# Performance work log

Hardware: AMD Instinct MI355X
Metric: run time of the kernel (lower is better)

Reference implementation:

```python
import jax, jax.numpy as jnp
import numpy as np

N_NODES = 50000
N_EDGES = 800000
IN_CH = 128
HEADS = 4
OUT_CH = 32
NEG_SLOPE = 0.2


def setup_inputs() -> dict:
    key = jax.random.key(0)
    ks = jax.random.split(key, 8)
    x = jax.random.normal(ks[0], (N_NODES, IN_CH), dtype=jnp.float32)
    # edges guaranteed to have no self-loops (module removes then re-adds them)
    tgt = jax.random.randint(ks[1], (N_EDGES,), 0, N_NODES)
    off = jax.random.randint(ks[2], (N_EDGES,), 1, N_NODES)
    src = (tgt + off) % N_NODES
    edge_index = jnp.stack([src, tgt]).astype(jnp.int64)
    glorot = lambda k, shp: jax.random.uniform(
        k, shp, jnp.float32, -1.0, 1.0) * np.sqrt(6.0 / (shp[-1] + shp[-2]))
    Wl = glorot(ks[3], (HEADS * OUT_CH, IN_CH))  # torch Linear weight [out,in]
    Wr = glorot(ks[4], (HEADS * OUT_CH, IN_CH))
    att = glorot(ks[5], (1, HEADS, OUT_CH))
    bl = jnp.zeros((HEADS * OUT_CH,), jnp.float32)
    br = jnp.zeros((HEADS * OUT_CH,), jnp.float32)
    bias = jnp.zeros((HEADS * OUT_CH,), jnp.float32)
    return {"x": x, "edge_index": edge_index, "Wl": Wl, "bl": bl,
            "Wr": Wr, "br": br, "att": att, "bias": bias}


def _forward(x, edge_index, Wl, bl, Wr, br, att, bias):
    H, C = HEADS, OUT_CH
    n = x.shape[0]
    x_l = (x @ Wl.T + bl).reshape(n, H, C)  # target projection
    x_r = (x @ Wr.T + br).reshape(n, H, C)  # source projection
    # add self-loops (inputs contain none by construction)
    loops = jnp.arange(n, dtype=edge_index.dtype)
    src = jnp.concatenate([edge_index[0], loops])
    tgt = jnp.concatenate([edge_index[1], loops])
    x_i = x_l[tgt]                     # [E', H, C]
    x_j = x_r[src]                     # [E', H, C]
    a_in = jax.nn.leaky_relu(x_i + x_j, NEG_SLOPE)
    alpha = jnp.einsum('ehc,ohc->eh', a_in, att)  # [E', H]
    # segment softmax over target nodes
    m = jax.ops.segment_max(alpha, tgt, num_segments=n)
    alpha = jnp.exp(alpha - jax.lax.stop_gradient(m)[tgt])
    denom = jax.ops.segment_sum(alpha, tgt, num_segments=n)
    alpha = alpha / denom[tgt]
    msgs = x_j * alpha[:, :, None]     # [E', H, C]
    out = jax.ops.segment_sum(msgs, tgt, num_segments=n)  # [N, H, C]
    out = out.reshape(n, H * C) + bias  # concat=True
    return out


def reference(x, edge_index, Wl, bl, Wr, br, att, bias):
    return _forward(x, edge_index, Wl, bl, Wr, br, att, bias)
```

## Files before the change

### kernel.cpp

```cpp
#include <hip/hip_runtime.h>
#include <hip/hip_bf16.h>
#include <stdint.h>

#define N_NODES 50000
#define N_EDGES 800000
#define IN_CH   128
#define NEG_SLOPE 0.2f

#define E_PER 8
#define FILL_BLOCKS 391

typedef short short8 __attribute__((ext_vector_type(8)));
typedef float f32x4  __attribute__((ext_vector_type(4)));
typedef float f32x2  __attribute__((ext_vector_type(2)));

static __device__ __forceinline__ float bf_lo(uint32_t p) { return __uint_as_float(p << 16); }
static __device__ __forceinline__ float bf_hi(uint32_t p) { return __uint_as_float(p & 0xffff0000u); }
static __device__ __forceinline__ uint16_t f_to_bf(float f) {
    uint32_t u = __float_as_uint(f);
    u += 0x7fffu + ((u >> 16) & 1u);
    return (uint16_t)(u >> 16);
}

static __device__ __forceinline__ f32x2 lrelu2(f32x2 x) {
    f32x2 s = x * NEG_SLOPE;
    f32x2 r;
    r[0] = fmaxf(x[0], s[0]);
    r[1] = fmaxf(x[1], s[1]);
    return r;
}

static __device__ __forceinline__ float sum16(float x) {
    x += __uint_as_float(__builtin_amdgcn_update_dpp(0, __float_as_uint(x), 0xB1,  0xf, 0xf, true));
    x += __uint_as_float(__builtin_amdgcn_update_dpp(0, __float_as_uint(x), 0x4E,  0xf, 0xf, true));
    x += __uint_as_float(__builtin_amdgcn_update_dpp(0, __float_as_uint(x), 0x141, 0xf, 0xf, true));
    x += __uint_as_float(__builtin_amdgcn_update_dpp(0, __float_as_uint(x), 0x140, 0xf, 0xf, true));
    return x;
}

static __device__ __forceinline__ void sum16x2(float& a, float& b) {
    asm("s_nop 0\n\t"
        "v_add_f32 %0, %0, %0 quad_perm:[1,0,3,2] row_mask:0xf bank_mask:0xf bound_ctrl:0\n\t"
        "v_add_f32 %1, %1, %1 quad_perm:[1,0,3,2] row_mask:0xf bank_mask:0xf bound_ctrl:0\n\t"
        "v_add_f32 %0, %0, %0 quad_perm:[2,3,0,1] row_mask:0xf bank_mask:0xf bound_ctrl:0\n\t"
        "v_add_f32 %1, %1, %1 quad_perm:[2,3,0,1] row_mask:0xf bank_mask:0xf bound_ctrl:0\n\t"
        "v_add_f32 %0, %0, %0 row_half_mirror row_mask:0xf bank_mask:0xf bound_ctrl:0\n\t"
        "v_add_f32 %1, %1, %1 row_half_mirror row_mask:0xf bank_mask:0xf bound_ctrl:0\n\t"
        "v_add_f32 %0, %0, %0 row_mirror row_mask:0xf bank_mask:0xf bound_ctrl:0\n\t"
        "v_add_f32 %1, %1, %1 row_mirror row_mask:0xf bank_mask:0xf bound_ctrl:0"
        : "+v"(a), "+v"(b));
}

__global__ __launch_bounds__(256) void prep_kernel(
    const float* __restrict__ Wl, const float* __restrict__ Wr,
    __hip_bfloat16* __restrict__ wswz, int* __restrict__ cnt)
{
    int t = blockIdx.x * 256 + threadIdx.x;
    if (t < 4096) {
        int ct = t >> 8, rem = t & 255;
        int ch = rem >> 6, lane = rem & 63;
        int m = lane & 15, quad = lane >> 4;
        const float* W = (ct < 8) ? Wl : Wr;
        int o = ((ct & 7) << 4) + m;
        const float* src = W + (size_t)o * IN_CH + ch * 32 + quad * 8;
        short8 f;
#pragma unroll
        for (int j = 0; j < 8; ++j) f[j] = (short)f_to_bf(src[j]);
        *(short8*)((short*)wswz + (size_t)t * 8) = f;
    }
    for (int i = t; i < N_NODES; i += 64 * 256) cnt[i] = 0;
}

__global__ __launch_bounds__(256) void fill_kernel(
    const int* __restrict__ ei, int cap,
    int* __restrict__ cnt, uint16_t* __restrict__ csr)
{
    const uint32_t* eiw = (const uint32_t*)ei;
    bool z = (eiw[2 * (threadIdx.x & 63) + 1] == 0u);
    bool is64 = __popcll(__ballot(z)) >= 32;

    int tid = blockIdx.x * 256 + threadIdx.x;
    int e0 = tid * E_PER;
    if (e0 >= N_EDGES) return;

    int src[E_PER], tgt[E_PER];
    if (is64) {
        const int4* ps = (const int4*)(eiw + 2 * (size_t)e0);
        const int4* pt = (const int4*)(eiw + 2 * ((size_t)N_EDGES + e0));
#pragma unroll
        for (int k = 0; k < 4; ++k) {
            int4 s = ps[k], t = pt[k];
            src[2 * k] = s.x; src[2 * k + 1] = s.z;
            tgt[2 * k] = t.x; tgt[2 * k + 1] = t.z;
        }
    } else {
        const int4* ps = (const int4*)(ei + e0);
        const int4* pt = (const int4*)(ei + N_EDGES + e0);
#pragma unroll
        for (int k = 0; k < 2; ++k) {
            int4 s = ps[k], t = pt[k];
            src[4 * k] = s.x; src[4 * k + 1] = s.y; src[4 * k + 2] = s.z; src[4 * k + 3] = s.w;
            tgt[4 * k] = t.x; tgt[4 * k + 1] = t.y; tgt[4 * k + 2] = t.z; tgt[4 * k + 3] = t.w;
        }
    }

    int pos[E_PER];
#pragma unroll
    for (int k = 0; k < E_PER; ++k) {
        bool ok = (unsigned)src[k] < N_NODES && (unsigned)tgt[k] < N_NODES;
        pos[k] = ok ? atomicAdd(&cnt[tgt[k]], 1) : cap;
    }
#pragma unroll
    for (int k = 0; k < E_PER; ++k)
        if (pos[k] < cap) csr[(size_t)tgt[k] * cap + pos[k]] = (uint16_t)src[k];
}

__global__ __launch_bounds__(256) void proj_kernel(
    const float* __restrict__ x, const __hip_bfloat16* __restrict__ wswz,
    const float* __restrict__ bl, const float* __restrict__ br,
    float* __restrict__ xl, __hip_bfloat16* __restrict__ xr)
{
    int rowbase = blockIdx.x * 16;
    int lane = threadIdx.x & 63;
    int widx = threadIdx.x >> 6;
    int m = lane & 15;
    int quad = lane >> 4;

    short8 afrag[4];
    const float* xrow = x + (size_t)(rowbase + m) * IN_CH;
#pragma unroll
    for (int ch = 0; ch < 4; ++ch) {
        f32x4 p0 = *(const f32x4*)(xrow + ch * 32 + quad * 8);
        f32x4 p1 = *(const f32x4*)(xrow + ch * 32 + quad * 8 + 4);
        short8 f;
#pragma unroll
        for (int j = 0; j < 4; ++j) { f[j] = (short)f_to_bf(p0[j]); f[j + 4] = (short)f_to_bf(p1[j]); }
        afrag[ch] = f;
    }

    const short* wz = (const short*)wswz;
    const float* bv = (widx < 2) ? bl : br;
#pragma unroll
    for (int cc = 0; cc < 4; ++cc) {
        int ct = widx * 4 + cc;
        int o = ((ct & 7) << 4) + m;
        f32x4 acc = {0.f, 0.f, 0.f, 0.f};
#pragma unroll
        for (int ch = 0; ch < 4; ++ch) {
            short8 bfrag = *(const short8*)(wz + ((size_t)(ct * 4 + ch) * 64 + lane) * 8);
            acc = __builtin_amdgcn_mfma_f32_16x16x32_bf16(afrag[ch], bfrag, acc, 0, 0, 0);
        }
        float bias_v = bv[o];
        if (widx < 2) {
#pragma unroll
            for (int r = 0; r < 4; ++r)
                xl[(size_t)(rowbase + quad * 4 + r) * IN_CH + o] = acc[r] + bias_v;
        } else {
#pragma unroll
            for (int r = 0; r < 4; ++r)
                xr[(size_t)(rowbase + quad * 4 + r) * IN_CH + o] = __float2bfloat16(acc[r] + bias_v);
        }
    }
}

__global__ __launch_bounds__(256) void agg_kernel(
    const __hip_bfloat16* __restrict__ xr,
    const int* __restrict__ cnt, const uint16_t* __restrict__ csr, int cap,
    const float* __restrict__ att, const float* __restrict__ bias,
    float* out )
{
    int n = blockIdx.x * 4 + (threadIdx.x >> 6);
    if (n >= N_NODES) return;
    int lane = threadIdx.x & 63;

    const uint32_t* xrw = (const uint32_t*)xr;

    f32x2 qv = *(const f32x2*)(out + (size_t)n * IN_CH + 2 * lane);
    f32x2 av = *(const f32x2*)(att + 2 * lane);
    f32x2 bv = *(const f32x2*)(bias + 2 * lane);

    int deg = min(cnt[n], cap);
    const uint16_t* lst = csr + (size_t)n * cap;
    int idxreg = (int)lst[min(lane, cap - 1)];

    uint32_t u = xrw[(size_t)n * 64 + lane];
    f32x2 a0v; a0v[0] = bf_lo(u); a0v[1] = bf_hi(u);
    f32x2 p0 = lrelu2(qv + a0v) * av;
    float t = sum16(p0[0] + p0[1]);
    float w = __expf(t);
    float lsum = w;
    f32x2 acc = w * a0v;

    if (deg > 0) {
        int dm1 = deg - 1;
        int s0a = __builtin_amdgcn_readlane(idxreg, 0);
        int s0b = __builtin_amdgcn_readlane(idxreg, min(1, dm1));
        int s1a = __builtin_amdgcn_readlane(idxreg, min(2, dm1));
        int s1b = __builtin_amdgcn_readlane(idxreg, min(3, dm1));
        uint32_t uA0 = xrw[(size_t)s0a * 64 + lane];
        uint32_t uB0 = xrw[(size_t)s0b * 64 + lane];
        uint32_t uA1 = xrw[(size_t)s1a * 64 + lane];
        uint32_t uB1 = xrw[(size_t)s1b * 64 + lane];
        int i = 0;
        while (i + 1 < deg) {
            int s2a = __builtin_amdgcn_readlane(idxreg, min(i + 4, dm1));
            int s2b = __builtin_amdgcn_readlane(idxreg, min(i + 5, dm1));
            uint32_t uA2 = xrw[(size_t)s2a * 64 + lane];
            uint32_t uB2 = xrw[(size_t)s2b * 64 + lane];

            f32x2 aA; aA[0] = bf_lo(uA0); aA[1] = bf_hi(uA0);
            f32x2 aB; aB[0] = bf_lo(uB0); aB[1] = bf_hi(uB0);
            f32x2 pA = lrelu2(qv + aA) * av;
            f32x2 pB = lrelu2(qv + aB) * av;
            float tA = pA[0] + pA[1];
            float tB = pB[0] + pB[1];
            sum16x2(tA, tB);
            float wA = __expf(tA), wB = __expf(tB);
            lsum += wA + wB;
            acc += wA * aA;
            acc += wB * aB;

            uA0 = uA1; uB0 = uB1;
            uA1 = uA2; uB1 = uB2;
            i += 2;
        }
        if (i < deg) {
            f32x2 aA; aA[0] = bf_lo(uA0); aA[1] = bf_hi(uA0);
            f32x2 pA = lrelu2(qv + aA) * av;
            float tA = sum16(pA[0] + pA[1]);
            float wA = __expf(tA);
            lsum += wA;
            acc += wA * aA;
        }
    }

    float inv = 1.f / lsum;
    f32x2 ov = acc * inv + bv;
    *(f32x2*)(out + (size_t)n * IN_CH + 2 * lane) = ov;
}

extern "C" void kernel_launch(void* const* d_in, const int* in_sizes, int n_in,
                              void* d_out, int out_size, void* d_ws, size_t ws_size,
                              hipStream_t stream) {
    const float* x    = (const float*)d_in[0];
    const int*   ei   = (const int*)d_in[1];
    const float* Wl   = (const float*)d_in[2];
    const float* bl   = (const float*)d_in[3];
    const float* Wr   = (const float*)d_in[4];
    const float* br   = (const float*)d_in[5];
    const float* att  = (const float*)d_in[6];
    const float* bias = (const float*)d_in[7];
    float* out = (float*)d_out;

    const size_t CSR_BASE = 13065536;
    char* ws = (char*)d_ws;
    __hip_bfloat16* xr   = (__hip_bfloat16*)(ws);
    __hip_bfloat16* wswz = (__hip_bfloat16*)(ws + 12800000);
    int*      cnt = (int*)(ws + 12865536);
    uint16_t* csr = (uint16_t*)(ws + CSR_BASE);

    long long avail = (ws_size > CSR_BASE) ? (long long)(ws_size - CSR_BASE) : 0;
    int cap = (int)(avail / ((long long)N_NODES * 2));
    if (cap > 64) cap = 64;
    if (cap < 1)  cap = 1;

    prep_kernel<<<64, 256, 0, stream>>>(Wl, Wr, wswz, cnt);
    fill_kernel<<<FILL_BLOCKS, 256, 0, stream>>>(ei, cap, cnt, csr);
    proj_kernel<<<N_NODES / 16, 256, 0, stream>>>(x, wswz, bl, br, out, xr);
    agg_kernel<<<N_NODES / 4, 256, 0, stream>>>(xr, cnt, csr, cap, att, bias, out);
}
```

Measured before the change: 190.9 us.

## Build CSR via bucketed two-pass sort fused with projection kernel

Replaces the global-atomic scatter CSR fill with a two-level bucket sort. Edges are histogrammed into 512-node buckets in shared memory and written to per-bucket regions, then a per-bucket kernel builds a compact CSR slab with packed 8-bit degrees in LDS. The fill blocks are fused into the projection kernel launch, so edge bucketing overlaps with the MFMA projection and one launch goes away. This aims to cut scattered global atomics and uncoalesced CSR writes. In exchange it needs extra workspace, caps per-bucket and per-node counts (BCAP, CAPR=48) that could drop edges on skewed graphs, and keeps the old path as a fallback.

```diff
diff --git a/kernel.cpp b/kernel.cpp
--- a/kernel.cpp
+++ b/kernel.cpp
@@ -6,6 +6,13 @@
 #define N_EDGES 800000
 #define IN_CH   128
 #define NEG_SLOPE 0.2f
+
+#define NBUCK   98
+#define E1      8000
+#define FILLB   100
+#define BCAP    12288
+#define BSTRIDE 49152
+#define CAPR    48
 
 #define E_PER 8
 #define FILL_BLOCKS 391
@@ -51,24 +58,176 @@
         : "+v"(a), "+v"(b));
 }
 
+static __device__ __forceinline__ void wswz_body(
+    int t, const float* __restrict__ Wl, const float* __restrict__ Wr,
+    __hip_bfloat16* __restrict__ wswz)
+{
+    int ct = t >> 8, rem = t & 255;
+    int ch = rem >> 6, lane = rem & 63;
+    int m = lane & 15, quad = lane >> 4;
+    const float* W = (ct < 8) ? Wl : Wr;
+    int o = ((ct & 7) << 4) + m;
+    const float* src = W + (size_t)o * IN_CH + ch * 32 + quad * 8;
+    short8 f;
+#pragma unroll
+    for (int j = 0; j < 8; ++j) f[j] = (short)f_to_bf(src[j]);
+    *(short8*)((short*)wswz + (size_t)t * 8) = f;
+}
+
+static __device__ __forceinline__ void proj_body(
+    int rowbase, int tid,
+    const float* __restrict__ x, const __hip_bfloat16* __restrict__ wswz,
+    const float* __restrict__ bl, const float* __restrict__ br,
+    float* __restrict__ xl, __hip_bfloat16* __restrict__ xr)
+{
+    int lane = tid & 63;
+    int widx = tid >> 6;
+    int m = lane & 15;
+    int quad = lane >> 4;
+
+    short8 afrag[4];
+    const float* xrow = x + (size_t)(rowbase + m) * IN_CH;
+#pragma unroll
+    for (int ch = 0; ch < 4; ++ch) {
+        f32x4 p0 = *(const f32x4*)(xrow + ch * 32 + quad * 8);
+        f32x4 p1 = *(const f32x4*)(xrow + ch * 32 + quad * 8 + 4);
+        short8 f;
+#pragma unroll
+        for (int j = 0; j < 4; ++j) { f[j] = (short)f_to_bf(p0[j]); f[j + 4] = (short)f_to_bf(p1[j]); }
+        afrag[ch] = f;
+    }
+
+    const short* wz = (const short*)wswz;
+    const float* bv = (widx < 2) ? bl : br;
+#pragma unroll
+    for (int cc = 0; cc < 4; ++cc) {
+        int ct = widx * 4 + cc;
+        int o = ((ct & 7) << 4) + m;
+        f32x4 acc = {0.f, 0.f, 0.f, 0.f};
+#pragma unroll
+        for (int ch = 0; ch < 4; ++ch) {
+            short8 bfrag = *(const short8*)(wz + ((size_t)(ct * 4 + ch) * 64 + lane) * 8);
+            acc = __builtin_amdgcn_mfma_f32_16x16x32_bf16(afrag[ch], bfrag, acc, 0, 0, 0);
+        }
+        float bias_v = bv[o];
+        if (widx < 2) {
+#pragma unroll
+            for (int r = 0; r < 4; ++r)
+                xl[(size_t)(rowbase + quad * 4 + r) * IN_CH + o] = acc[r] + bias_v;
+        } else {
+#pragma unroll
+            for (int r = 0; r < 4; ++r)
+                xr[(size_t)(rowbase + quad * 4 + r) * IN_CH + o] = __float2bfloat16(acc[r] + bias_v);
+        }
+    }
+}
+
 __global__ __launch_bounds__(256) void prep_kernel(
     const float* __restrict__ Wl, const float* __restrict__ Wr,
-    __hip_bfloat16* __restrict__ wswz, int* __restrict__ cnt)
+    __hip_bfloat16* __restrict__ wswz, int* __restrict__ z, int zn)
 {
     int t = blockIdx.x * 256 + threadIdx.x;
-    if (t < 4096) {
-        int ct = t >> 8, rem = t & 255;
-        int ch = rem >> 6, lane = rem & 63;
-        int m = lane & 15, quad = lane >> 4;
-        const float* W = (ct < 8) ? Wl : Wr;
-        int o = ((ct & 7) << 4) + m;
-        const float* src = W + (size_t)o * IN_CH + ch * 32 + quad * 8;
-        short8 f;
-#pragma unroll
-        for (int j = 0; j < 8; ++j) f[j] = (short)f_to_bf(src[j]);
-        *(short8*)((short*)wswz + (size_t)t * 8) = f;
-    }
-    for (int i = t; i < N_NODES; i += 64 * 256) cnt[i] = 0;
+    if (t < 4096) wswz_body(t, Wl, Wr, wswz);
+    for (int i = t; i < zn; i += 64 * 256) z[i] = 0;
+}
+
+__global__ __launch_bounds__(256) void proj_fill(
+    const float* __restrict__ x, const __hip_bfloat16* __restrict__ wswz,
+    const float* __restrict__ bl, const float* __restrict__ br,
+    float* __restrict__ xl, __hip_bfloat16* __restrict__ xr,
+    const int* __restrict__ ei, uint32_t* __restrict__ bcnt,
+    char* __restrict__ region)
+{
+    __shared__ uint32_t s_sorted[E1];
+    __shared__ uint32_t s_hist[NBUCK], s_lstart[NBUCK], s_loc[NBUCK], s_gbase[NBUCK];
+    __shared__ uint32_t s_T;
+
+    if (blockIdx.x >= FILLB) {
+        proj_body((blockIdx.x - FILLB) * 16, threadIdx.x, x, wswz, bl, br, xl, xr);
+        return;
+    }
+
+    int tid = threadIdx.x;
+    int fb = blockIdx.x;
+    for (int i = tid; i < NBUCK; i += 256) s_hist[i] = 0;
+    __syncthreads();
+
+    const uint32_t* eiw = (const uint32_t*)ei;
+    bool zlo = (eiw[2 * (tid & 63) + 1] == 0u);
+    bool is64 = __popcll(__ballot(zlo)) >= 32;
+    int e0 = fb * E1;
+
+    for (int k = tid; k < E1; k += 256) {
+        int e = e0 + k;
+        int s = is64 ? (int)eiw[2 * (size_t)e] : ei[e];
+        int t = is64 ? (int)eiw[2 * ((size_t)N_EDGES + e)] : ei[N_EDGES + e];
+        if ((unsigned)s < N_NODES && (unsigned)t < N_NODES)
+            atomicAdd(&s_hist[t >> 9], 1u);
+    }
+    __syncthreads();
+
+    if (tid < NBUCK) s_gbase[tid] = atomicAdd(&bcnt[tid], s_hist[tid]);
+    if (tid == 0) {
+        uint32_t acc = 0;
+        for (int i = 0; i < NBUCK; ++i) { s_lstart[i] = acc; acc += s_hist[i]; }
+        s_T = acc;
+    }
+    __syncthreads();
+    if (tid < NBUCK) s_loc[tid] = s_lstart[tid];
+    __syncthreads();
+
+    for (int k = tid; k < E1; k += 256) {
+        int e = e0 + k;
+        int s = is64 ? (int)eiw[2 * (size_t)e] : ei[e];
+        int t = is64 ? (int)eiw[2 * ((size_t)N_EDGES + e)] : ei[N_EDGES + e];
+        if ((unsigned)s < N_NODES && (unsigned)t < N_NODES) {
+            uint32_t r = atomicAdd(&s_loc[t >> 9], 1u);
+            s_sorted[r] = ((uint32_t)t << 16) | (uint32_t)s;
+        }
+    }
+    __syncthreads();
+
+    int T = (int)s_T;
+    for (int k = tid; k < T; k += 256) {
+        uint32_t v = s_sorted[k];
+        uint32_t key = v >> 25;
+        uint32_t g = s_gbase[key] + (uint32_t)k - s_lstart[key];
+        if (g < BCAP)
+            ((uint32_t*)(region + (size_t)key * BSTRIDE))[g] = v;
+    }
+}
+
+__global__ __launch_bounds__(256) void csr_build(
+    const uint32_t* __restrict__ bcnt, char* __restrict__ region,
+    uint32_t* __restrict__ degs32)
+{
+    __shared__ uint16_t slab[512 * CAPR];
+    __shared__ uint32_t lcnt[512];
+    int b = blockIdx.x, tid = threadIdx.x;
+    for (int i = tid; i < 512; i += 256) lcnt[i] = 0;
+    __syncthreads();
+
+    uint32_t* reg = (uint32_t*)(region + (size_t)b * BSTRIDE);
+    int M = min((int)bcnt[b], BCAP);
+    for (int k = tid; k < M; k += 256) {
+        uint32_t v = reg[k];
+        int node = (int)((v >> 16) & 511u);
+        uint32_t pos = atomicAdd(&lcnt[node], 1u);
+        if (pos < CAPR) slab[node * CAPR + pos] = (uint16_t)(v & 0xffffu);
+    }
+    __syncthreads();
+
+    const uint32_t* sw = (const uint32_t*)slab;
+    for (int j = tid; j < (512 * CAPR / 2); j += 256) reg[j] = sw[j];
+    if (tid < 128) {
+        uint32_t p = 0;
+#pragma unroll
+        for (int q = 0; q < 4; ++q) {
+            uint32_t d = min(lcnt[tid * 4 + q], (uint32_t)CAPR);
+            p |= d << (q * 8);
+        }
+        degs32[b * 128 + tid] = p;
+    }
 }
 
 __global__ __launch_bounds__(256) void fill_kernel(
@@ -120,52 +279,13 @@
     const float* __restrict__ bl, const float* __restrict__ br,
     float* __restrict__ xl, __hip_bfloat16* __restrict__ xr)
 {
-    int rowbase = blockIdx.x * 16;
-    int lane = threadIdx.x & 63;
-    int widx = threadIdx.x >> 6;
-    int m = lane & 15;
-    int quad = lane >> 4;
-
-    short8 afrag[4];
-    const float* xrow = x + (size_t)(rowbase + m) * IN_CH;
-#pragma unroll
-    for (int ch = 0; ch < 4; ++ch) {
-        f32x4 p0 = *(const f32x4*)(xrow + ch * 32 + quad * 8);
-        f32x4 p1 = *(const f32x4*)(xrow + ch * 32 + quad * 8 + 4);
-        short8 f;
-#pragma unroll
-        for (int j = 0; j < 4; ++j) { f[j] = (short)f_to_bf(p0[j]); f[j + 4] = (short)f_to_bf(p1[j]); }
-        afrag[ch] = f;
-    }
-
-    const short* wz = (const short*)wswz;
-    const float* bv = (widx < 2) ? bl : br;
-#pragma unroll
-    for (int cc = 0; cc < 4; ++cc) {
-        int ct = widx * 4 + cc;
-        int o = ((ct & 7) << 4) + m;
-        f32x4 acc = {0.f, 0.f, 0.f, 0.f};
-#pragma unroll
-        for (int ch = 0; ch < 4; ++ch) {
-            short8 bfrag = *(const short8*)(wz + ((size_t)(ct * 4 + ch) * 64 + lane) * 8);
-            acc = __builtin_amdgcn_mfma_f32_16x16x32_bf16(afrag[ch], bfrag, acc, 0, 0, 0);
-        }
-        float bias_v = bv[o];
-        if (widx < 2) {
-#pragma unroll
-            for (int r = 0; r < 4; ++r)
-                xl[(size_t)(rowbase + quad * 4 + r) * IN_CH + o] = acc[r] + bias_v;
-        } else {
-#pragma unroll
-            for (int r = 0; r < 4; ++r)
-                xr[(size_t)(rowbase + quad * 4 + r) * IN_CH + o] = __float2bfloat16(acc[r] + bias_v);
-        }
-    }
+    proj_body(blockIdx.x * 16, threadIdx.x, x, wswz, bl, br, xl, xr);
 }
 
 __global__ __launch_bounds__(256) void agg_kernel(
     const __hip_bfloat16* __restrict__ xr,
-    const int* __restrict__ cnt, const uint16_t* __restrict__ csr, int cap,
+    const char* __restrict__ degbase, int degpacked,
+    const uint16_t* __restrict__ csr, int ldcsr, int cap,
     const float* __restrict__ att, const float* __restrict__ bias,
     float* out )
 {
@@ -179,8 +299,16 @@
     f32x2 av = *(const f32x2*)(att + 2 * lane);
     f32x2 bv = *(const f32x2*)(bias + 2 * lane);
 
-    int deg = min(cnt[n], cap);
-    const uint16_t* lst = csr + (size_t)n * cap;
+    int deg;
+    if (degpacked) {
+        uint32_t pk = ((const uint32_t*)degbase)[n >> 2];
+        deg = (int)((pk >> ((n & 3) * 8)) & 255u);
+    } else {
+        deg = ((const int*)degbase)[n];
+    }
+    deg = min(deg, cap);
+
+    const uint16_t* lst = csr + (size_t)n * ldcsr;
     int idxreg = (int)lst[min(lane, cap - 1)];
 
     uint32_t u = xrw[(size_t)n * 64 + lane];
@@ -252,20 +380,40 @@
     const float* bias = (const float*)d_in[7];
     float* out = (float*)d_out;
 
-    const size_t CSR_BASE = 13065536;
     char* ws = (char*)d_ws;
     __hip_bfloat16* xr   = (__hip_bfloat16*)(ws);
     __hip_bfloat16* wswz = (__hip_bfloat16*)(ws + 12800000);
-    int*      cnt = (int*)(ws + 12865536);
-    uint16_t* csr = (uint16_t*)(ws + CSR_BASE);
-
-    long long avail = (ws_size > CSR_BASE) ? (long long)(ws_size - CSR_BASE) : 0;
-    int cap = (int)(avail / ((long long)N_NODES * 2));
-    if (cap > 64) cap = 64;
-    if (cap < 1)  cap = 1;
-
-    prep_kernel<<<64, 256, 0, stream>>>(Wl, Wr, wswz, cnt);
-    fill_kernel<<<FILL_BLOCKS, 256, 0, stream>>>(ei, cap, cnt, csr);
-    proj_kernel<<<N_NODES / 16, 256, 0, stream>>>(x, wswz, bl, br, out, xr);
-    agg_kernel<<<N_NODES / 4, 256, 0, stream>>>(xr, cnt, csr, cap, att, bias, out);
-}
+
+    const size_t DEGS_OFF = 12865536;
+    const size_t BCNT_OFF = 12915712;
+    const size_t REG_OFF  = 12916224;
+    const size_t NEED     = REG_OFF + (size_t)NBUCK * BSTRIDE;
+
+    if (ws_size >= NEED) {
+        uint32_t* degs   = (uint32_t*)(ws + DEGS_OFF);
+        uint32_t* bcnt   = (uint32_t*)(ws + BCNT_OFF);
+        char*     region = ws + REG_OFF;
+
+        prep_kernel<<<64, 256, 0, stream>>>(Wl, Wr, wswz, (int*)bcnt, 128);
+        proj_fill<<<FILLB + N_NODES / 16, 256, 0, stream>>>(
+            x, wswz, bl, br, out, xr, ei, bcnt, region);
+        csr_build<<<NBUCK, 256, 0, stream>>>(bcnt, region, degs);
+        agg_kernel<<<N_NODES / 4, 256, 0, stream>>>(
+            xr, (const char*)degs, 1, (const uint16_t*)region, CAPR, CAPR,
+            att, bias, out);
+    } else {
+        const size_t CSR_BASE = 13065536;
+        int*      cnt = (int*)(ws + 12865536);
+        uint16_t* csr = (uint16_t*)(ws + CSR_BASE);
+        long long avail = (ws_size > CSR_BASE) ? (long long)(ws_size - CSR_BASE) : 0;
+        int cap = (int)(avail / ((long long)N_NODES * 2));
+        if (cap > 64) cap = 64;
+        if (cap < 1)  cap = 1;
+
+        prep_kernel<<<64, 256, 0, stream>>>(Wl, Wr, wswz, cnt, N_NODES);
+        fill_kernel<<<FILL_BLOCKS, 256, 0, stream>>>(ei, cap, cnt, csr);
+        proj_kernel<<<N_NODES / 16, 256, 0, stream>>>(x, wswz, bl, br, out, xr);
+        agg_kernel<<<N_NODES / 4, 256, 0, stream>>>(
+            xr, (const char*)cnt, 0, csr, cap, cap, att, bias, out);
+    }
+}
```

Measured after the change: 177.5 us. 7.0% less time.
